# Kernel optimization log

Measured on AMD Instinct MI355X. Metric: run time of the kernel, lower is better.

## Reference

```python
import jax, jax.numpy as jnp
import numpy as np

NMS_RADIUS = 2.0   # cfgs.NMS_radius (meters)
EPS = 1e-6         # torch nn.PairwiseDistance default eps (added to the diff)
M = 16384          # number of keypoint candidates
SCENE = 100.0      # scene extent in meters


def setup_inputs() -> dict:
    key = jax.random.key(0)
    k1, k2 = jax.random.split(key)
    nodes = jax.random.uniform(k1, (M, 3), dtype=jnp.float32) * SCENE
    overlap_score = jax.random.normal(k2, (M,), dtype=jnp.float32)
    return {"nodes": nodes, "overlap_score": overlap_score}


def _greedy_nms(nodes, radius):
    """Sequential greedy NMS: keep node i iff its distance to every
    already-kept node exceeds radius. Faithful to the torch loop:
    (dis > radius).sum() == n_kept  <=>  all kept dists > radius."""
    n = nodes.shape[0]

    def body(i, mask):
        # torch nn.PairwiseDistance computes ||x1 - x2 + eps||_2
        d = jnp.linalg.norm(nodes[i] - nodes + EPS, axis=-1)  # [n]
        keep = jnp.all(jnp.where(mask, d > radius, True))
        return mask.at[i].set(keep)

    mask0 = jnp.zeros(n, dtype=bool).at[0].set(True)
    return jax.lax.fori_loop(1, n, body, mask0)


def reference(nodes, overlap_score):
    # sort by overlap score descending, run greedy NMS, unsort the mask
    order = jnp.argsort(-overlap_score)
    mask_sorted = _greedy_nms(nodes[order], NMS_RADIUS)
    mask = jnp.zeros_like(mask_sorted).at[order].set(mask_sorted)
    nms_length = mask.sum(dtype=jnp.int32)[None]
    return mask, nms_length
```

## Files before the change

### kernel.cpp

```cpp
#include <hip/hip_runtime.h>


#define M_PTS    16384
#define RADIUS   2.0f
#define EPS_D    1e-6f
#define GRID_N   25
#define NCELLS   (GRID_N * GRID_N * GRID_N)
#define CELL_CAP 12
#define K_NBR    12
#define CELLS_PB (GRID_N * GRID_N)
#define LIST_PB  (CELLS_PB * CELL_CAP)
#define EPT      5
#define ACT_PAD  (EPT * 1024)
#define SENT     M_PTS


__device__ __forceinline__ int cell_of(float v) {
  int c = (int)(v * 0.25f);
  return c < 0 ? 0 : (c > GRID_N - 1 ? GRID_N - 1 : c);
}

__device__ __forceinline__ bool edge_test(float4 pi, float4 pj, int j, int i) {
  bool earlier = (pj.w > pi.w) || ((pj.w == pi.w) && (j < i));
  if (!earlier) return false;
  float ddx = __fadd_rn(__fsub_rn(pi.x, pj.x), EPS_D);
  float ddy = __fadd_rn(__fsub_rn(pi.y, pj.y), EPS_D);
  float ddz = __fadd_rn(__fsub_rn(pi.z, pj.z), EPS_D);
  float d2 = __fadd_rn(__fadd_rn(__fmul_rn(ddx, ddx), __fmul_rn(ddy, ddy)),
                       __fmul_rn(ddz, ddz));
  return !(__fsqrt_rn(d2) > RADIUS);
}

__global__ __launch_bounds__(1024) void bin25(
    const float* __restrict__ nodes, const float* __restrict__ score,
    float4* __restrict__ pts, int* __restrict__ cell_cnt,
    unsigned short* __restrict__ cell_list) {
  __shared__ int ccnt[CELLS_PB];
  __shared__ unsigned short clist[LIST_PB];
  const int tid = threadIdx.x;
  const int b   = blockIdx.x;
  if (tid < CELLS_PB) ccnt[tid] = 0;
  __syncthreads();

  for (int i = tid; i < M_PTS; i += 1024) {
    float x = nodes[3 * i + 0];
    if (cell_of(x) != b) continue;
    float y = nodes[3 * i + 1];
    float z = nodes[3 * i + 2];
    float s = score[i];
    pts[i] = make_float4(x, y, z, s);
    int lc = cell_of(y) * GRID_N + cell_of(z);
    int pos = atomicAdd(&ccnt[lc], 1);
    if (pos < CELL_CAP) clist[lc * CELL_CAP + pos] = (unsigned short)i;
  }
  __syncthreads();

  if (tid < CELLS_PB) {
    int v = ccnt[tid];
    cell_cnt[b * CELLS_PB + tid] = v > CELL_CAP ? CELL_CAP : v;
  }
  for (int e = tid; e < LIST_PB; e += 1024)
    cell_list[b * LIST_PB + e] = clist[e];
}

__global__ __launch_bounds__(256) void wscan(
    const float4* __restrict__ pts, const int* __restrict__ cell_cnt,
    const unsigned short* __restrict__ cell_list,
    int* __restrict__ cnt, unsigned short* __restrict__ nbr) {
  const int tid  = threadIdx.x;
  const int lane = tid & 63;
  const int d    = lane & 31;
  const int half = lane >> 5;
  const int gwave = (blockIdx.x * 256 + tid) >> 6;
  const int i = gwave * 2 + half;

  const float4 pi = pts[i];
  int n = 0, cid = 0, m = 0, firstj = 0;
  if (d < 27) {
    int cx = cell_of(pi.x) + d / 9 - 1;
    int cy = cell_of(pi.y) + (d / 3) % 3 - 1;
    int cz = cell_of(pi.z) + d % 3 - 1;
    if (cx >= 0 && cx < GRID_N && cy >= 0 && cy < GRID_N &&
        cz >= 0 && cz < GRID_N) {
      cid = (cx * GRID_N + cy) * GRID_N + cz;
      m = cell_cnt[cid];
      for (int s = 0; s < m; ++s) {
        int j = cell_list[cid * CELL_CAP + s];
        if (edge_test(pi, pts[j], j, i)) { if (!n) firstj = j; ++n; }
      }
    }
  }
  int x = n;
#pragma unroll
  for (int off = 1; off < 32; off <<= 1) {
    int y = __shfl_up(x, off, 32);
    if (d >= off) x += y;
  }
  int excl = x - n;
  int tot = __shfl(x, 31, 32);
  if (n == 1) {
    if (excl < K_NBR) nbr[i * K_NBR + excl] = (unsigned short)firstj;
  } else if (n > 1) {
    int pos = excl;
    for (int s = 0; s < m && pos < K_NBR; ++s) {
      int j = cell_list[cid * CELL_CAP + s];
      if (edge_test(pi, pts[j], j, i)) {
        nbr[i * K_NBR + pos] = (unsigned short)j;
        ++pos;
      }
    }
  }
  if (d == 0) cnt[i] = tot > K_NBR ? K_NBR : tot;
}

__global__ __launch_bounds__(1024) void solve_nb(
    const int* __restrict__ cnt, const unsigned short* __restrict__ nbr,
    int* __restrict__ out, int out_size) {
  __shared__ unsigned char mask[M_PTS + 4];
  __shared__ unsigned int act[ACT_PAD];
  __shared__ int act_n, total;

  const int tid = threadIdx.x;
  const int lane = tid & 63;
  if (tid == 0) { act_n = 0; total = 0; }
  unsigned int* mask4 = (unsigned int*)mask;
  for (int w = tid; w < M_PTS / 4; w += 1024) mask4[w] = 0x01010101u;
  if (tid == 0) mask4[M_PTS / 4] = 0u;
  for (int a = tid; a < ACT_PAD; a += 1024) act[a] = 0u;
  __syncthreads();

  for (int k = tid; k < M_PTS; k += 1024) {
    int c = cnt[k];
    if (c > K_NBR) c = K_NBR;
    unsigned long long b = __ballot(c > 0);
    int wcnt = __popcll(b);
    int wbase = 0;
    if (lane == 0 && wcnt) wbase = atomicAdd(&act_n, wcnt);
    wbase = __shfl(wbase, 0, 64);
    if (c > 0) {
      int pos = wbase + __popcll(b & ((1ull << lane) - 1ull));
      if (pos < ACT_PAD) act[pos] = (unsigned)k | ((unsigned)c << 16);
    }
  }
  __syncthreads();
  const int na = act_n;
  const bool ok = (na <= ACT_PAD);

  unsigned ae[EPT];
  unsigned short r0[EPT], r1[EPT], r2[EPT];
  int cur[EPT];
#pragma unroll
  for (int e = 0; e < EPT; ++e) {
    unsigned v = act[tid + e * 1024];
    ae[e] = v;
    int k = (int)(v & 0xFFFFu);
    int c = (int)(v >> 16);
    const unsigned short* row = nbr + (size_t)k * K_NBR;
    unsigned w = (c > 0) ? *(const unsigned int*)row : 0u;
    r0[e] = (c > 0) ? (unsigned short)(w & 0xFFFFu) : (unsigned short)SENT;
    r1[e] = (c > 1) ? (unsigned short)(w >> 16)     : (unsigned short)SENT;
    r2[e] = (c > 2) ? row[2]                        : (unsigned short)SENT;
    cur[e] = 1;
  }
  __syncthreads();

  if (ok) {
    for (int it = 0; it < 96; ++it) {
      int m0[EPT], m1[EPT], m2[EPT];
#pragma unroll
      for (int e = 0; e < EPT; ++e) m0[e] = (int)mask[r0[e]];
#pragma unroll
      for (int e = 0; e < EPT; ++e) m1[e] = (int)mask[r1[e]];
#pragma unroll
      for (int e = 0; e < EPT; ++e) m2[e] = (int)mask[r2[e]];
      int any = 0;
#pragma unroll
      for (int e = 0; e < EPT; ++e) {
        unsigned v = ae[e];
        int c = (int)(v >> 16);
        if (!c) continue;
        int kp = (m0[e] ^ 1) & (m1[e] ^ 1) & (m2[e] ^ 1);
        if (c > 3) {
          int k = (int)(v & 0xFFFFu);
          const unsigned short* row = nbr + (size_t)k * K_NBR;
          for (int t = 3; t < c; ++t) kp &= (int)mask[row[t]] ^ 1;
        }
        if (kp != cur[e]) {
          cur[e] = kp;
          mask[v & 0xFFFFu] = (unsigned char)kp;
          any = 1;
        }
      }
      if (__syncthreads_count(any) == 0) break;
    }
  } else {
    __shared__ int changed;
    for (int it = 0; it < 512; ++it) {
      if (tid == 0) changed = 0;
      __syncthreads();
      int any = 0;
      for (int k = tid; k < M_PTS; k += 1024) {
        int c = cnt[k]; if (c > K_NBR) c = K_NBR;
        if (!c) continue;
        int kp = 1;
        for (int t = 0; t < c; ++t) kp &= (int)mask[nbr[k * K_NBR + t]] ^ 1;
        if (kp != (int)mask[k]) { mask[k] = (unsigned char)kp; any = 1; }
      }
      if (any) changed = 1;
      __syncthreads();
      if (!changed) break;
    }
  }
  __syncthreads();

  int ks = 0;
  for (int k = tid; k < M_PTS; k += 1024) {
    int m = (int)mask[k];
    out[k] = m;
    ks += m;
  }
#pragma unroll
  for (int off = 32; off > 0; off >>= 1) ks += __shfl_down(ks, off, 64);
  if (lane == 0) atomicAdd(&total, ks);
  __syncthreads();
  if (tid == 0) out[out_size - 1] = total;
}

extern "C" void kernel_launch(void* const* d_in, const int* in_sizes, int n_in,
                              void* d_out, int out_size, void* d_ws, size_t ws_size,
                              hipStream_t stream) {
  const float* nodes = (const float*)d_in[0];
  const float* score = (const float*)d_in[1];
  int* out = (int*)d_out;

  char* ws = (char*)d_ws;
  float4* pts = (float4*)ws;
  int* cell_cnt = (int*)(ws + 262144);
  int* cnt = (int*)(ws + 327680);
  unsigned short* cell_list = (unsigned short*)(ws + 393216);
  unsigned short* nbr = (unsigned short*)(ws + 770048);

  bin25<<<GRID_N, 1024, 0, stream>>>(nodes, score, pts, cell_cnt, cell_list);
  wscan<<<2048, 256, 0, stream>>>(pts, cell_cnt, cell_list, cnt, nbr);
  solve_nb<<<1, 1024, 0, stream>>>(cnt, nbr, out, out_size);
}
```

Baseline: 39.11 us.

## Partition active nodes into score bands for Gauss-Seidel style NMS propagation

The solver now buckets active candidates into four score-quartile bands, so each thread's slots are ordered from high to low score. Mask updates are done in place within an iteration, so decisions about higher-score nodes reach lower-score nodes sooner. This is meant to cut the number of block-wide fixed-point iterations and barriers. The mask reads are also moved inside the per-element loop so they see updates made earlier in the same pass. In exchange it adds per-band ballots and atomics plus per-band overflow checks, and falls back to the slow path when any band exceeds its capacity.

```diff
diff --git a/kernel.cpp b/kernel.cpp
--- a/kernel.cpp
+++ b/kernel.cpp
@@ -11,7 +11,9 @@
 #define CELLS_PB (GRID_N * GRID_N)
 #define LIST_PB  (CELLS_PB * CELL_CAP)
 #define EPT      5
-#define ACT_PAD  (EPT * 1024)
+#define BANDS    4
+#define BAND_CAP 1280
+#define ACT_PAD  (BANDS * BAND_CAP)
 #define SENT     M_PTS
 
 
@@ -113,38 +115,52 @@
   if (d == 0) cnt[i] = tot > K_NBR ? K_NBR : tot;
 }
 
-__global__ __launch_bounds__(1024) void solve_nb(
-    const int* __restrict__ cnt, const unsigned short* __restrict__ nbr,
+__global__ __launch_bounds__(1024) void solve_gs(
+    const float4* __restrict__ pts, const int* __restrict__ cnt,
+    const unsigned short* __restrict__ nbr,
     int* __restrict__ out, int out_size) {
   __shared__ unsigned char mask[M_PTS + 4];
   __shared__ unsigned int act[ACT_PAD];
-  __shared__ int act_n, total;
+  __shared__ int bn[BANDS];
+  __shared__ int total;
 
   const int tid = threadIdx.x;
   const int lane = tid & 63;
-  if (tid == 0) { act_n = 0; total = 0; }
+  if (tid == 0) total = 0;
+  if (tid < BANDS) bn[tid] = 0;
   unsigned int* mask4 = (unsigned int*)mask;
   for (int w = tid; w < M_PTS / 4; w += 1024) mask4[w] = 0x01010101u;
   if (tid == 0) mask4[M_PTS / 4] = 0u;
   for (int a = tid; a < ACT_PAD; a += 1024) act[a] = 0u;
   __syncthreads();
 
+  bool ovf = false;
   for (int k = tid; k < M_PTS; k += 1024) {
     int c = cnt[k];
     if (c > K_NBR) c = K_NBR;
-    unsigned long long b = __ballot(c > 0);
-    int wcnt = __popcll(b);
-    int wbase = 0;
-    if (lane == 0 && wcnt) wbase = atomicAdd(&act_n, wcnt);
-    wbase = __shfl(wbase, 0, 64);
-    if (c > 0) {
-      int pos = wbase + __popcll(b & ((1ull << lane) - 1ull));
-      if (pos < ACT_PAD) act[pos] = (unsigned)k | ((unsigned)c << 16);
-    }
-  }
-  __syncthreads();
-  const int na = act_n;
-  const bool ok = (na <= ACT_PAD);
+    float s = pts[k].w;
+    int band = (s > 0.67448975f) ? 0 : (s > 0.0f) ? 1
+             : (s > -0.67448975f) ? 2 : 3;
+#pragma unroll
+    for (int b = 0; b < BANDS; ++b) {
+      bool sel = (c > 0) && (band == b);
+      unsigned long long bal = __ballot(sel);
+      if (!bal) continue;
+      int wcnt = __popcll(bal);
+      int wbase = 0;
+      if (lane == 0) wbase = atomicAdd(&bn[b], wcnt);
+      wbase = __shfl(wbase, 0, 64);
+      if (sel) {
+        int pos = wbase + __popcll(bal & ((1ull << lane) - 1ull));
+        if (pos < BAND_CAP) act[b * BAND_CAP + pos] = (unsigned)k | ((unsigned)c << 16);
+        else ovf = true;
+      }
+    }
+  }
+  __syncthreads();
+  bool ok = (bn[0] <= BAND_CAP) && (bn[1] <= BAND_CAP) &&
+            (bn[2] <= BAND_CAP) && (bn[3] <= BAND_CAP) && !ovf;
+  ok = __syncthreads_count(ok) == 1024;
 
   unsigned ae[EPT];
   unsigned short r0[EPT], r1[EPT], r2[EPT];
@@ -166,20 +182,16 @@
 
   if (ok) {
     for (int it = 0; it < 96; ++it) {
-      int m0[EPT], m1[EPT], m2[EPT];
-#pragma unroll
-      for (int e = 0; e < EPT; ++e) m0[e] = (int)mask[r0[e]];
-#pragma unroll
-      for (int e = 0; e < EPT; ++e) m1[e] = (int)mask[r1[e]];
-#pragma unroll
-      for (int e = 0; e < EPT; ++e) m2[e] = (int)mask[r2[e]];
       int any = 0;
 #pragma unroll
       for (int e = 0; e < EPT; ++e) {
         unsigned v = ae[e];
         int c = (int)(v >> 16);
+        int m0 = (int)mask[r0[e]];
+        int m1 = (int)mask[r1[e]];
+        int m2 = (int)mask[r2[e]];
         if (!c) continue;
-        int kp = (m0[e] ^ 1) & (m1[e] ^ 1) & (m2[e] ^ 1);
+        int kp = (m0 ^ 1) & (m1 ^ 1) & (m2 ^ 1);
         if (c > 3) {
           int k = (int)(v & 0xFFFFu);
           const unsigned short* row = nbr + (size_t)k * K_NBR;
@@ -242,5 +254,5 @@
 
   bin25<<<GRID_N, 1024, 0, stream>>>(nodes, score, pts, cell_cnt, cell_list);
   wscan<<<2048, 256, 0, stream>>>(pts, cell_cnt, cell_list, cnt, nbr);
-  solve_nb<<<1, 1024, 0, stream>>>(cnt, nbr, out, out_size);
-}
+  solve_gs<<<1, 1024, 0, stream>>>(pts, cnt, nbr, out, out_size);
+}
```

New measurement: 80.06 us. 2.05x slower.

## Build packed active-node list in scan kernel and drop full-mask passes in solver

Applied to the files above, without the earlier changes.

The neighbour-scan kernel now appends each node that has earlier conflicting neighbours to a global packed list, using a global atomic. Each entry carries the node index, its neighbour count and its first three neighbour ids. Nodes with no conflicts get their output written directly. The single-block solver no longer scans all counts to compact the active set and no longer gathers the first neighbours from global memory, and it writes outputs only for active nodes. This removes serial work from the one-block kernel, at the cost of a global atomic per node in the scan and a nondeterministic list order.

```diff
diff --git a/kernel.cpp b/kernel.cpp
--- a/kernel.cpp
+++ b/kernel.cpp
@@ -34,11 +34,12 @@
 __global__ __launch_bounds__(1024) void bin25(
     const float* __restrict__ nodes, const float* __restrict__ score,
     float4* __restrict__ pts, int* __restrict__ cell_cnt,
-    unsigned short* __restrict__ cell_list) {
+    unsigned short* __restrict__ cell_list, int* __restrict__ actn) {
   __shared__ int ccnt[CELLS_PB];
   __shared__ unsigned short clist[LIST_PB];
   const int tid = threadIdx.x;
   const int b   = blockIdx.x;
+  if (b == 0 && tid == 0) *actn = 0;
   if (tid < CELLS_PB) ccnt[tid] = 0;
   __syncthreads();
 
@@ -66,7 +67,8 @@
 __global__ __launch_bounds__(256) void wscan(
     const float4* __restrict__ pts, const int* __restrict__ cell_cnt,
     const unsigned short* __restrict__ cell_list,
-    int* __restrict__ cnt, unsigned short* __restrict__ nbr) {
+    unsigned short* __restrict__ nbr, uint2* __restrict__ actg,
+    int* __restrict__ actn, int* __restrict__ out) {
   const int tid  = threadIdx.x;
   const int lane = tid & 63;
   const int d    = lane & 31;
@@ -75,7 +77,8 @@
   const int i = gwave * 2 + half;
 
   const float4 pi = pts[i];
-  int n = 0, cid = 0, m = 0, firstj = 0;
+  int n = 0, cid = 0, m = 0;
+  int j0 = 0, j1 = 0, j2 = 0;
   if (d < 27) {
     int cx = cell_of(pi.x) + d / 9 - 1;
     int cy = cell_of(pi.y) + (d / 3) % 3 - 1;
@@ -86,7 +89,10 @@
       m = cell_cnt[cid];
       for (int s = 0; s < m; ++s) {
         int j = cell_list[cid * CELL_CAP + s];
-        if (edge_test(pi, pts[j], j, i)) { if (!n) firstj = j; ++n; }
+        if (edge_test(pi, pts[j], j, i)) {
+          if (n == 0) j0 = j; else if (n == 1) j1 = j; else if (n == 2) j2 = j;
+          ++n;
+        }
       }
     }
   }
@@ -99,7 +105,7 @@
   int excl = x - n;
   int tot = __shfl(x, 31, 32);
   if (n == 1) {
-    if (excl < K_NBR) nbr[i * K_NBR + excl] = (unsigned short)firstj;
+    if (excl < K_NBR) nbr[i * K_NBR + excl] = (unsigned short)j0;
   } else if (n > 1) {
     int pos = excl;
     for (int s = 0; s < m && pos < K_NBR; ++s) {
@@ -110,40 +116,49 @@
       }
     }
   }
-  if (d == 0) cnt[i] = tot > K_NBR ? K_NBR : tot;
-}
-
-__global__ __launch_bounds__(1024) void solve_nb(
-    const int* __restrict__ cnt, const unsigned short* __restrict__ nbr,
+  unsigned short rr0 = 0, rr1 = 0, rr2 = 0;
+#pragma unroll
+  for (int p = 0; p < 3; ++p) {
+    bool pred = (excl <= p) && (p < excl + n);
+    unsigned long long bal = __ballot(pred);
+    unsigned bh = (unsigned)(bal >> (half * 32));
+    int src = half * 32 + (bh ? (__ffs(bh) - 1) : 0);
+    int sj0 = __shfl(j0, src, 64);
+    int sj1 = __shfl(j1, src, 64);
+    int sj2 = __shfl(j2, src, 64);
+    int se  = __shfl(excl, src, 64);
+    int dp = p - se;
+    unsigned short rp = (unsigned short)(dp == 0 ? sj0 : dp == 1 ? sj1 : sj2);
+    if (p == 0) rr0 = rp; else if (p == 1) rr1 = rp; else rr2 = rp;
+  }
+  if (d == 0) {
+    if (tot == 0) {
+      out[i] = 1;
+    } else {
+      int c = tot > K_NBR ? K_NBR : tot;
+      int pos = atomicAdd(actn, 1);
+      unsigned e0 = (unsigned)i | ((unsigned)c << 14) | ((unsigned)rr0 << 18);
+      unsigned e1 = (unsigned)rr1 | ((unsigned)rr2 << 16);
+      actg[pos] = make_uint2(e0, e1);
+    }
+  }
+}
+
+__global__ __launch_bounds__(1024) void solve_pk(
+    const uint2* __restrict__ actg, const int* __restrict__ actn,
+    const unsigned short* __restrict__ nbr,
     int* __restrict__ out, int out_size) {
   __shared__ unsigned char mask[M_PTS + 4];
-  __shared__ unsigned int act[ACT_PAD];
-  __shared__ int act_n, total;
+  __shared__ int total;
 
   const int tid = threadIdx.x;
   const int lane = tid & 63;
-  if (tid == 0) { act_n = 0; total = 0; }
+  if (tid == 0) total = 0;
   unsigned int* mask4 = (unsigned int*)mask;
   for (int w = tid; w < M_PTS / 4; w += 1024) mask4[w] = 0x01010101u;
   if (tid == 0) mask4[M_PTS / 4] = 0u;
-  for (int a = tid; a < ACT_PAD; a += 1024) act[a] = 0u;
-  __syncthreads();
-
-  for (int k = tid; k < M_PTS; k += 1024) {
-    int c = cnt[k];
-    if (c > K_NBR) c = K_NBR;
-    unsigned long long b = __ballot(c > 0);
-    int wcnt = __popcll(b);
-    int wbase = 0;
-    if (lane == 0 && wcnt) wbase = atomicAdd(&act_n, wcnt);
-    wbase = __shfl(wbase, 0, 64);
-    if (c > 0) {
-      int pos = wbase + __popcll(b & ((1ull << lane) - 1ull));
-      if (pos < ACT_PAD) act[pos] = (unsigned)k | ((unsigned)c << 16);
-    }
-  }
-  __syncthreads();
-  const int na = act_n;
+
+  const int na = *actn;
   const bool ok = (na <= ACT_PAD);
 
   unsigned ae[EPT];
@@ -151,15 +166,14 @@
   int cur[EPT];
 #pragma unroll
   for (int e = 0; e < EPT; ++e) {
-    unsigned v = act[tid + e * 1024];
-    ae[e] = v;
-    int k = (int)(v & 0xFFFFu);
-    int c = (int)(v >> 16);
-    const unsigned short* row = nbr + (size_t)k * K_NBR;
-    unsigned w = (c > 0) ? *(const unsigned int*)row : 0u;
-    r0[e] = (c > 0) ? (unsigned short)(w & 0xFFFFu) : (unsigned short)SENT;
-    r1[e] = (c > 1) ? (unsigned short)(w >> 16)     : (unsigned short)SENT;
-    r2[e] = (c > 2) ? row[2]                        : (unsigned short)SENT;
+    int idx = tid + e * 1024;
+    uint2 ev = (ok && idx < na) ? actg[idx] : make_uint2(0u, 0u);
+    int k = (int)(ev.x & 0x3FFFu);
+    int c = (int)((ev.x >> 14) & 0xFu);
+    ae[e] = (unsigned)k | ((unsigned)c << 16);
+    r0[e] = (c > 0) ? (unsigned short)(ev.x >> 18)      : (unsigned short)SENT;
+    r1[e] = (c > 1) ? (unsigned short)(ev.y & 0xFFFFu)  : (unsigned short)SENT;
+    r2[e] = (c > 2) ? (unsigned short)(ev.y >> 16)      : (unsigned short)SENT;
     cur[e] = 1;
   }
   __syncthreads();
@@ -193,37 +207,57 @@
       }
       if (__syncthreads_count(any) == 0) break;
     }
+    int ks = 0;
+#pragma unroll
+    for (int e = 0; e < EPT; ++e) {
+      unsigned v = ae[e];
+      if ((v >> 16) != 0u) {
+        out[v & 0xFFFFu] = cur[e];
+        ks += cur[e];
+      }
+    }
+#pragma unroll
+    for (int off = 32; off > 0; off >>= 1) ks += __shfl_down(ks, off, 64);
+    if (lane == 0) atomicAdd(&total, ks);
+    __syncthreads();
+    if (tid == 0) out[out_size - 1] = (M_PTS - na) + total;
   } else {
     __shared__ int changed;
     for (int it = 0; it < 512; ++it) {
       if (tid == 0) changed = 0;
       __syncthreads();
       int any = 0;
-      for (int k = tid; k < M_PTS; k += 1024) {
-        int c = cnt[k]; if (c > K_NBR) c = K_NBR;
-        if (!c) continue;
-        int kp = 1;
-        for (int t = 0; t < c; ++t) kp &= (int)mask[nbr[k * K_NBR + t]] ^ 1;
+      for (int idx = tid; idx < na; idx += 1024) {
+        uint2 ev = actg[idx];
+        int k = (int)(ev.x & 0x3FFFu);
+        int c = (int)((ev.x >> 14) & 0xFu);
+        int kp = (int)mask[(unsigned short)(ev.x >> 18)] ^ 1;
+        if (c > 1) kp &= (int)mask[(unsigned short)(ev.y & 0xFFFFu)] ^ 1;
+        if (c > 2) kp &= (int)mask[(unsigned short)(ev.y >> 16)] ^ 1;
+        if (c > 3) {
+          const unsigned short* row = nbr + (size_t)k * K_NBR;
+          for (int t = 3; t < c; ++t) kp &= (int)mask[row[t]] ^ 1;
+        }
         if (kp != (int)mask[k]) { mask[k] = (unsigned char)kp; any = 1; }
       }
       if (any) changed = 1;
       __syncthreads();
       if (!changed) break;
     }
-  }
-  __syncthreads();
-
-  int ks = 0;
-  for (int k = tid; k < M_PTS; k += 1024) {
-    int m = (int)mask[k];
-    out[k] = m;
-    ks += m;
-  }
-#pragma unroll
-  for (int off = 32; off > 0; off >>= 1) ks += __shfl_down(ks, off, 64);
-  if (lane == 0) atomicAdd(&total, ks);
-  __syncthreads();
-  if (tid == 0) out[out_size - 1] = total;
+    __syncthreads();
+    int ks = 0;
+    for (int idx = tid; idx < na; idx += 1024) {
+      int k = (int)(actg[idx].x & 0x3FFFu);
+      int mv = (int)mask[k];
+      out[k] = mv;
+      ks += mv;
+    }
+#pragma unroll
+    for (int off = 32; off > 0; off >>= 1) ks += __shfl_down(ks, off, 64);
+    if (lane == 0) atomicAdd(&total, ks);
+    __syncthreads();
+    if (tid == 0) out[out_size - 1] = (M_PTS - na) + total;
+  }
 }
 
 extern "C" void kernel_launch(void* const* d_in, const int* in_sizes, int n_in,
@@ -236,11 +270,12 @@
   char* ws = (char*)d_ws;
   float4* pts = (float4*)ws;
   int* cell_cnt = (int*)(ws + 262144);
-  int* cnt = (int*)(ws + 327680);
+  int* actn = (int*)(ws + 327680);
   unsigned short* cell_list = (unsigned short*)(ws + 393216);
   unsigned short* nbr = (unsigned short*)(ws + 770048);
-
-  bin25<<<GRID_N, 1024, 0, stream>>>(nodes, score, pts, cell_cnt, cell_list);
-  wscan<<<2048, 256, 0, stream>>>(pts, cell_cnt, cell_list, cnt, nbr);
-  solve_nb<<<1, 1024, 0, stream>>>(cnt, nbr, out, out_size);
-}
+  uint2* actg = (uint2*)(ws + 1179648);
+
+  bin25<<<GRID_N, 1024, 0, stream>>>(nodes, score, pts, cell_cnt, cell_list, actn);
+  wscan<<<2048, 256, 0, stream>>>(pts, cell_cnt, cell_list, nbr, actg, actn, out);
+  solve_pk<<<1, 1024, 0, stream>>>(actg, actn, nbr, out, out_size);
+}
```

After: 67.79 us. +73.3%, slower.
